# Performance work log

Hardware: AMD Instinct MI355X
Metric: run time of the kernel (lower is better)

Reference implementation:

```python
import jax, jax.numpy as jnp
import numpy as np

B, NT, DIM, H = 8, 1024, 768, 12
HD = DIM // H
SCALE = HD ** -0.5


def setup_inputs() -> dict:
    key = jax.random.key(0)
    ks = jax.random.split(key, 9)
    s = DIM ** -0.5
    return {
        "tfeat": jax.random.normal(ks[0], (B, NT, DIM), jnp.float32),
        "wq": jax.random.normal(ks[1], (DIM, DIM), jnp.float32) * s,
        "bq": jnp.zeros((DIM,), jnp.float32),
        "wk": jax.random.normal(ks[2], (DIM, DIM), jnp.float32) * s,
        "bk": jnp.zeros((DIM,), jnp.float32),
        "wv": jax.random.normal(ks[3], (DIM, DIM), jnp.float32) * s,
        "bv": jnp.zeros((DIM,), jnp.float32),
        "wp": jax.random.normal(ks[4], (DIM, DIM), jnp.float32) * s,
        "bp": jnp.zeros((DIM,), jnp.float32),
    }


def reference(tfeat, wq, bq, wk, bk, wv, bv, wp, bp):
    # Linear stores weight [out, in]; y = x @ W^T + b
    def split_heads(x):  # [B,Nt,C] -> [B,H,Nt,hd]
        b, n, c = x.shape
        return x.reshape(b, n, H, HD).transpose(0, 2, 1, 3)

    q = split_heads(tfeat @ wq.T + bq)
    k = split_heads(tfeat @ wk.T + bk)
    v = split_heads(tfeat @ wv.T + bv)
    # [B,H,Nt,Nt]
    attn = jax.nn.softmax(jnp.einsum('bhqd,bhkd->bhqk', q, k) * SCALE, axis=-1)
    # dropout is identity in eval mode
    x = jnp.einsum('bhqk,bhkd->bhqd', attn, v)
    x = x.transpose(0, 2, 1, 3).reshape(tfeat.shape)
    x = x @ wp.T + bp
    return (x, attn)
```

## Files before the change

### kernel.cpp

```cpp
#include <hip/hip_runtime.h>
#include <hip/hip_bf16.h>
#include <math.h>

#define B_    8
#define NT_   1024
#define DIM_  768
#define H_    12
#define HD_   64
#define SCALE_ 0.125f

typedef _Float16 half8  __attribute__((ext_vector_type(8)));
typedef float    floatx4 __attribute__((ext_vector_type(4)));

__global__ void cvt_f32_f16(const float* __restrict__ in,
                            _Float16* __restrict__ out, int n) {
  int i = blockIdx.x * 256 + threadIdx.x;
  if (i < n) out[i] = (_Float16)in[i];
}

template<bool F32OUT>
__global__ __launch_bounds__(256) void gemm_bt(
    const _Float16* __restrict__ A, const _Float16* __restrict__ Bt,
    const float* __restrict__ bias, _Float16* __restrict__ outh,
    float* __restrict__ outf, int M, int N, int K)
{
  __shared__ _Float16 As[64][40];
  __shared__ _Float16 Bs[64][40];
  const int t    = threadIdx.x;
  const int w    = t >> 6, lane = t & 63;
  const int quad = lane >> 4, l16 = lane & 15;
  const int wm   = (w >> 1) * 32, wn = (w & 1) * 32;
  const int m0   = blockIdx.x * 64, n0 = blockIdx.y * 64;
  const int lrow = t >> 2, lcol = (t & 3) * 8;

  floatx4 acc[2][2] = {};

  for (int k0 = 0; k0 < K; k0 += 32) {
    uint4 av = *(const uint4*)(A  + (size_t)(m0 + lrow) * K + k0 + lcol);
    uint4 bv = *(const uint4*)(Bt + (size_t)(n0 + lrow) * K + k0 + lcol);
    __syncthreads();
    *(uint4*)(&As[lrow][lcol]) = av;
    *(uint4*)(&Bs[lrow][lcol]) = bv;
    __syncthreads();
    half8 a0 = *(const half8*)(&As[wm      + l16][quad * 8]);
    half8 a1 = *(const half8*)(&As[wm + 16 + l16][quad * 8]);
    half8 b0 = *(const half8*)(&Bs[wn      + l16][quad * 8]);
    half8 b1 = *(const half8*)(&Bs[wn + 16 + l16][quad * 8]);
    acc[0][0] = __builtin_amdgcn_mfma_f32_16x16x32_f16(a0, b0, acc[0][0], 0, 0, 0);
    acc[0][1] = __builtin_amdgcn_mfma_f32_16x16x32_f16(a0, b1, acc[0][1], 0, 0, 0);
    acc[1][0] = __builtin_amdgcn_mfma_f32_16x16x32_f16(a1, b0, acc[1][0], 0, 0, 0);
    acc[1][1] = __builtin_amdgcn_mfma_f32_16x16x32_f16(a1, b1, acc[1][1], 0, 0, 0);
  }

  for (int i = 0; i < 2; i++)
    for (int j = 0; j < 2; j++)
      for (int r = 0; r < 4; r++) {
        int row = m0 + wm + i * 16 + quad * 4 + r;
        int col = n0 + wn + j * 16 + l16;
        float v = acc[i][j][r] + bias[col];
        if (F32OUT) outf[(size_t)row * N + col] = v;
        else        outh[(size_t)row * N + col] = (_Float16)v;
      }
}

__global__ __launch_bounds__(256) void attn_kernel(
    const _Float16* __restrict__ Qh, const _Float16* __restrict__ Kh,
    const _Float16* __restrict__ Vh, float* __restrict__ attn_out,
    _Float16* __restrict__ Xh)
{
  __shared__ _Float16 Qs[64][72];
  __shared__ _Float16 Ks[64][72];
  __shared__ _Float16 Vt[64][72];
  __shared__ _Float16 Ps[64][72];

  const int t    = threadIdx.x;
  const int w    = t >> 6, lane = t & 63;
  const int quad = lane >> 4, l16 = lane & 15;
  const int qt = blockIdx.x, h = blockIdx.y, b = blockIdx.z;
  const int q0 = qt * 64;

  const _Float16* Qb = Qh + ((size_t)b * NT_) * DIM_ + h * HD_;
  const _Float16* Kb = Kh + ((size_t)b * NT_) * DIM_ + h * HD_;
  const _Float16* Vb = Vh + ((size_t)b * NT_) * DIM_ + h * HD_;

  const int lrow = t >> 2;
  const int lcol = (t & 3) * 16;

  *(uint4*)(&Qs[lrow][lcol])     = *(const uint4*)(Qb + (size_t)(q0 + lrow) * DIM_ + lcol);
  *(uint4*)(&Qs[lrow][lcol + 8]) = *(const uint4*)(Qb + (size_t)(q0 + lrow) * DIM_ + lcol + 8);

  float m_run[4], l_run[4];
#pragma unroll
  for (int r = 0; r < 4; r++) { m_run[r] = -INFINITY; l_run[r] = 0.0f; }

  for (int kt = 0; kt < 16; kt++) {
    __syncthreads();
    *(uint4*)(&Ks[lrow][lcol])     = *(const uint4*)(Kb + (size_t)(kt * 64 + lrow) * DIM_ + lcol);
    *(uint4*)(&Ks[lrow][lcol + 8]) = *(const uint4*)(Kb + (size_t)(kt * 64 + lrow) * DIM_ + lcol + 8);
    __syncthreads();

    floatx4 s[4] = {};
#pragma unroll
    for (int ks = 0; ks < 2; ks++) {
      half8 a = *(const half8*)(&Qs[w * 16 + l16][ks * 32 + quad * 8]);
#pragma unroll
      for (int j = 0; j < 4; j++) {
        half8 bk = *(const half8*)(&Ks[j * 16 + l16][ks * 32 + quad * 8]);
        s[j] = __builtin_amdgcn_mfma_f32_16x16x32_f16(a, bk, s[j], 0, 0, 0);
      }
    }
#pragma unroll
    for (int r = 0; r < 4; r++) {
      float tm = -INFINITY;
#pragma unroll
      for (int j = 0; j < 4; j++) tm = fmaxf(tm, s[j][r] * SCALE_);
      for (int off = 1; off < 16; off <<= 1)
        tm = fmaxf(tm, __shfl_xor(tm, off, 64));
      float nm = fmaxf(m_run[r], tm);
      float ts = 0.0f;
#pragma unroll
      for (int j = 0; j < 4; j++) ts += expf(s[j][r] * SCALE_ - nm);
      for (int off = 1; off < 16; off <<= 1)
        ts += __shfl_xor(ts, off, 64);
      l_run[r] = l_run[r] * expf(m_run[r] - nm) + ts;
      m_run[r] = nm;
    }
  }

  float inv_l[4];
#pragma unroll
  for (int r = 0; r < 4; r++) inv_l[r] = 1.0f / l_run[r];

  floatx4 oacc[4] = {};
  float* attn_b = attn_out + ((size_t)(b * H_ + h) * NT_ + q0) * NT_;

  for (int kt = 0; kt < 16; kt++) {
    __syncthreads();
    *(uint4*)(&Ks[lrow][lcol])     = *(const uint4*)(Kb + (size_t)(kt * 64 + lrow) * DIM_ + lcol);
    *(uint4*)(&Ks[lrow][lcol + 8]) = *(const uint4*)(Kb + (size_t)(kt * 64 + lrow) * DIM_ + lcol + 8);
    {
      alignas(16) _Float16 vh[16];
      *(uint4*)(vh)     = *(const uint4*)(Vb + (size_t)(kt * 64 + lrow) * DIM_ + lcol);
      *(uint4*)(vh + 8) = *(const uint4*)(Vb + (size_t)(kt * 64 + lrow) * DIM_ + lcol + 8);
#pragma unroll
      for (int c = 0; c < 16; c++) Vt[lcol + c][lrow] = vh[c];
    }
    __syncthreads();

    floatx4 s[4] = {};
#pragma unroll
    for (int ks = 0; ks < 2; ks++) {
      half8 a = *(const half8*)(&Qs[w * 16 + l16][ks * 32 + quad * 8]);
#pragma unroll
      for (int j = 0; j < 4; j++) {
        half8 bk = *(const half8*)(&Ks[j * 16 + l16][ks * 32 + quad * 8]);
        s[j] = __builtin_amdgcn_mfma_f32_16x16x32_f16(a, bk, s[j], 0, 0, 0);
      }
    }

#pragma unroll
    for (int j = 0; j < 4; j++)
#pragma unroll
      for (int r = 0; r < 4; r++) {
        float p = expf(s[j][r] * SCALE_ - m_run[r]) * inv_l[r];
        int qr = w * 16 + quad * 4 + r;
        attn_b[(size_t)qr * NT_ + kt * 64 + j * 16 + l16] = p;
        Ps[qr][j * 16 + l16] = (_Float16)p;
      }

#pragma unroll
    for (int ks = 0; ks < 2; ks++) {
      half8 pa = *(const half8*)(&Ps[w * 16 + l16][ks * 32 + quad * 8]);
#pragma unroll
      for (int j2 = 0; j2 < 4; j2++) {
        half8 bv = *(const half8*)(&Vt[j2 * 16 + l16][ks * 32 + quad * 8]);
        oacc[j2] = __builtin_amdgcn_mfma_f32_16x16x32_f16(pa, bv, oacc[j2], 0, 0, 0);
      }
    }
  }

#pragma unroll
  for (int j2 = 0; j2 < 4; j2++)
#pragma unroll
    for (int r = 0; r < 4; r++) {
      int qr = q0 + w * 16 + quad * 4 + r;
      Xh[((size_t)b * NT_ + qr) * DIM_ + h * HD_ + j2 * 16 + l16] = (_Float16)oacc[j2][r];
    }
}

extern "C" void kernel_launch(void* const* d_in, const int* in_sizes, int n_in,
                              void* d_out, int out_size, void* d_ws, size_t ws_size,
                              hipStream_t stream) {
  const float* tfeat = (const float*)d_in[0];
  const float* wq    = (const float*)d_in[1];
  const float* bq    = (const float*)d_in[2];
  const float* wk    = (const float*)d_in[3];
  const float* bk    = (const float*)d_in[4];
  const float* wv    = (const float*)d_in[5];
  const float* bv    = (const float*)d_in[6];
  const float* wp    = (const float*)d_in[7];
  const float* bp    = (const float*)d_in[8];
  float* out = (float*)d_out;

  const size_t T = (size_t)B_ * NT_ * DIM_;
  const size_t W = (size_t)DIM_ * DIM_;

  _Float16* ws  = (_Float16*)d_ws;
  _Float16* tfh = ws;
  _Float16* wqh = ws + T;
  _Float16* wkh = ws + T + W;
  _Float16* wvh = ws + T + 2 * W;
  _Float16* wph = ws + T + 3 * W;
  _Float16* Qh  = ws + T + 4 * W;
  _Float16* Kh  = Qh + T;
  _Float16* Vh  = Kh + T;
  _Float16* Xh  = Vh + T;

  cvt_f32_f16<<<(int)((T + 255) / 256), 256, 0, stream>>>(tfeat, tfh, (int)T);
  cvt_f32_f16<<<(int)((W + 255) / 256), 256, 0, stream>>>(wq, wqh, (int)W);
  cvt_f32_f16<<<(int)((W + 255) / 256), 256, 0, stream>>>(wk, wkh, (int)W);
  cvt_f32_f16<<<(int)((W + 255) / 256), 256, 0, stream>>>(wv, wvh, (int)W);
  cvt_f32_f16<<<(int)((W + 255) / 256), 256, 0, stream>>>(wp, wph, (int)W);

  dim3 gg(8192 / 64, 768 / 64);
  gemm_bt<false><<<gg, 256, 0, stream>>>(tfh, wqh, bq, Qh, nullptr, 8192, 768, 768);
  gemm_bt<false><<<gg, 256, 0, stream>>>(tfh, wkh, bk, Kh, nullptr, 8192, 768, 768);
  gemm_bt<false><<<gg, 256, 0, stream>>>(tfh, wvh, bv, Vh, nullptr, 8192, 768, 768);

  attn_kernel<<<dim3(NT_ / 64, H_, B_), 256, 0, stream>>>(Qh, Kh, Vh, out + T, Xh);

  gemm_bt<true><<<gg, 256, 0, stream>>>(Xh, wph, bp, nullptr, out, 8192, 768, 768);
}
```

Before: 711.4 us.

## Fuse QKV GEMMs into 128x128 LDS-DMA GEMM, exp2 softmax, vectorized casts

Replaces the 64x64 GEMM with a 128x128-tile kernel that loads global data straight into LDS through global_load_lds, and merges the Q, K and V projections into one launch by relying on the contiguous workspace layout of wq/wk/wv. The attention kernel now keeps Q fragments in registers instead of LDS. Softmax uses exp2 with a prescaled log2e constant and folds 1/l into the exponent via log2(l). The f32-to-f16 casts are vectorized to four elements per thread. Together these aim to cut launch count, raise GEMM data reuse and reduce transcendental cost, at the price of more registers and an unpadded LDS layout that may cause bank conflicts.

```diff
diff --git a/kernel.cpp b/kernel.cpp
--- a/kernel.cpp
+++ b/kernel.cpp
@@ -1,5 +1,4 @@
 #include <hip/hip_runtime.h>
-#include <hip/hip_bf16.h>
 #include <math.h>
 
 #define B_    8
@@ -8,59 +7,99 @@
 #define H_    12
 #define HD_   64
 #define SCALE_ 0.125f
+#define T_ELEMS 6291456UL
 
 typedef _Float16 half8  __attribute__((ext_vector_type(8)));
+typedef _Float16 half4v __attribute__((ext_vector_type(4)));
 typedef float    floatx4 __attribute__((ext_vector_type(4)));
 
-__global__ void cvt_f32_f16(const float* __restrict__ in,
-                            _Float16* __restrict__ out, int n) {
+#if __has_builtin(__builtin_amdgcn_exp2f)
+#define EXP2F(x) __builtin_amdgcn_exp2f(x)
+#else
+#define EXP2F(x) exp2f(x)
+#endif
+
+#define GLD16(gp, lp) __builtin_amdgcn_global_load_lds( \
+    (const __attribute__((address_space(1))) unsigned int*)(gp), \
+    (__attribute__((address_space(3))) unsigned int*)(lp), 16, 0, 0)
+
+__global__ void cvt4(const float* __restrict__ in, _Float16* __restrict__ out,
+                     int n4) {
   int i = blockIdx.x * 256 + threadIdx.x;
-  if (i < n) out[i] = (_Float16)in[i];
-}
-
-template<bool F32OUT>
-__global__ __launch_bounds__(256) void gemm_bt(
+  if (i < n4) {
+    float4 v = ((const float4*)in)[i];
+    half4v h = { (_Float16)v.x, (_Float16)v.y, (_Float16)v.z, (_Float16)v.w };
+    *(half4v*)(out + 4 * (size_t)i) = h;
+  }
+}
+
+template<int MODE>
+__global__ __launch_bounds__(256) void gemm128(
     const _Float16* __restrict__ A, const _Float16* __restrict__ Bt,
-    const float* __restrict__ bias, _Float16* __restrict__ outh,
-    float* __restrict__ outf, int M, int N, int K)
+    const float* __restrict__ b0_, const float* __restrict__ b1_,
+    const float* __restrict__ b2_, _Float16* __restrict__ outh,
+    float* __restrict__ outf, int K)
 {
-  __shared__ _Float16 As[64][40];
-  __shared__ _Float16 Bs[64][40];
+  __shared__ _Float16 As[128 * 32];
+  __shared__ _Float16 Bs[128 * 32];
   const int t    = threadIdx.x;
   const int w    = t >> 6, lane = t & 63;
   const int quad = lane >> 4, l16 = lane & 15;
-  const int wm   = (w >> 1) * 32, wn = (w & 1) * 32;
-  const int m0   = blockIdx.x * 64, n0 = blockIdx.y * 64;
-  const int lrow = t >> 2, lcol = (t & 3) * 8;
-
-  floatx4 acc[2][2] = {};
+  const int wm   = (w >> 1) * 64, wn = (w & 1) * 64;
+  const int m0   = blockIdx.x * 128, n0 = blockIdx.y * 128;
+
+  const _Float16* gA = A  + (size_t)(m0 + (t >> 2)) * K + (t & 3) * 8;
+  const _Float16* gB = Bt + (size_t)(n0 + (t >> 2)) * K + (t & 3) * 8;
+  _Float16* lA = As + w * 512;
+  _Float16* lB = Bs + w * 512;
+  const size_t rowK = (size_t)64 * K;
+
+  floatx4 acc[4][4] = {};
 
   for (int k0 = 0; k0 < K; k0 += 32) {
-    uint4 av = *(const uint4*)(A  + (size_t)(m0 + lrow) * K + k0 + lcol);
-    uint4 bv = *(const uint4*)(Bt + (size_t)(n0 + lrow) * K + k0 + lcol);
-    __syncthreads();
-    *(uint4*)(&As[lrow][lcol]) = av;
-    *(uint4*)(&Bs[lrow][lcol]) = bv;
-    __syncthreads();
-    half8 a0 = *(const half8*)(&As[wm      + l16][quad * 8]);
-    half8 a1 = *(const half8*)(&As[wm + 16 + l16][quad * 8]);
-    half8 b0 = *(const half8*)(&Bs[wn      + l16][quad * 8]);
-    half8 b1 = *(const half8*)(&Bs[wn + 16 + l16][quad * 8]);
-    acc[0][0] = __builtin_amdgcn_mfma_f32_16x16x32_f16(a0, b0, acc[0][0], 0, 0, 0);
-    acc[0][1] = __builtin_amdgcn_mfma_f32_16x16x32_f16(a0, b1, acc[0][1], 0, 0, 0);
-    acc[1][0] = __builtin_amdgcn_mfma_f32_16x16x32_f16(a1, b0, acc[1][0], 0, 0, 0);
-    acc[1][1] = __builtin_amdgcn_mfma_f32_16x16x32_f16(a1, b1, acc[1][1], 0, 0, 0);
-  }
-
-  for (int i = 0; i < 2; i++)
-    for (int j = 0; j < 2; j++)
+    __syncthreads();
+    GLD16(gA + k0,        lA);
+    GLD16(gA + rowK + k0, lA + 2048);
+    GLD16(gB + k0,        lB);
+    GLD16(gB + rowK + k0, lB + 2048);
+    __syncthreads();
+
+    half8 af[4], bf[4];
+#pragma unroll
+    for (int i = 0; i < 4; i++)
+      af[i] = *(const half8*)(As + (wm + i * 16 + l16) * 32 + quad * 8);
+#pragma unroll
+    for (int j = 0; j < 4; j++)
+      bf[j] = *(const half8*)(Bs + (wn + j * 16 + l16) * 32 + quad * 8);
+#pragma unroll
+    for (int i = 0; i < 4; i++)
+#pragma unroll
+      for (int j = 0; j < 4; j++)
+        acc[i][j] = __builtin_amdgcn_mfma_f32_16x16x32_f16(af[i], bf[j],
+                                                           acc[i][j], 0, 0, 0);
+  }
+
+  const int sel = (MODE == 0) ? (n0 / 768) : 0;
+  const float* bb = (MODE == 0)
+                      ? (sel == 0 ? b0_ : (sel == 1 ? b1_ : b2_))
+                      : b0_;
+#pragma unroll
+  for (int j = 0; j < 4; j++) {
+    const int col = n0 + wn + j * 16 + l16;
+    const int cl  = col - sel * 768;
+    const float bv = bb[cl];
+#pragma unroll
+    for (int i = 0; i < 4; i++)
+#pragma unroll
       for (int r = 0; r < 4; r++) {
-        int row = m0 + wm + i * 16 + quad * 4 + r;
-        int col = n0 + wn + j * 16 + l16;
-        float v = acc[i][j][r] + bias[col];
-        if (F32OUT) outf[(size_t)row * N + col] = v;
-        else        outh[(size_t)row * N + col] = (_Float16)v;
-      }
+        const int row = m0 + wm + i * 16 + quad * 4 + r;
+        const float v = acc[i][j][r] + bv;
+        if (MODE == 0)
+          outh[(size_t)sel * T_ELEMS + (size_t)row * 768 + cl] = (_Float16)v;
+        else
+          outf[(size_t)row * 768 + col] = v;
+      }
+  }
 }
 
 __global__ __launch_bounds__(256) void attn_kernel(
@@ -68,7 +107,6 @@
     const _Float16* __restrict__ Vh, float* __restrict__ attn_out,
     _Float16* __restrict__ Xh)
 {
-  __shared__ _Float16 Qs[64][72];
   __shared__ _Float16 Ks[64][72];
   __shared__ _Float16 Vt[64][72];
   __shared__ _Float16 Ps[64][72];
@@ -86,9 +124,14 @@
   const int lrow = t >> 2;
   const int lcol = (t & 3) * 16;
 
-  *(uint4*)(&Qs[lrow][lcol])     = *(const uint4*)(Qb + (size_t)(q0 + lrow) * DIM_ + lcol);
-  *(uint4*)(&Qs[lrow][lcol + 8]) = *(const uint4*)(Qb + (size_t)(q0 + lrow) * DIM_ + lcol + 8);
-
+  half8 qf[2];
+  {
+    const _Float16* qr = Qb + (size_t)(q0 + w * 16 + l16) * DIM_ + quad * 8;
+    qf[0] = *(const half8*)(qr);
+    qf[1] = *(const half8*)(qr + 32);
+  }
+
+  const float C2 = 0.18033688011112042f;
   float m_run[4], l_run[4];
 #pragma unroll
   for (int r = 0; r < 4; r++) { m_run[r] = -INFINITY; l_run[r] = 0.0f; }
@@ -102,34 +145,31 @@
     floatx4 s[4] = {};
 #pragma unroll
     for (int ks = 0; ks < 2; ks++) {
-      half8 a = *(const half8*)(&Qs[w * 16 + l16][ks * 32 + quad * 8]);
 #pragma unroll
       for (int j = 0; j < 4; j++) {
         half8 bk = *(const half8*)(&Ks[j * 16 + l16][ks * 32 + quad * 8]);
-        s[j] = __builtin_amdgcn_mfma_f32_16x16x32_f16(a, bk, s[j], 0, 0, 0);
+        s[j] = __builtin_amdgcn_mfma_f32_16x16x32_f16(qf[ks], bk, s[j], 0, 0, 0);
       }
     }
 #pragma unroll
     for (int r = 0; r < 4; r++) {
-      float tm = -INFINITY;
-#pragma unroll
-      for (int j = 0; j < 4; j++) tm = fmaxf(tm, s[j][r] * SCALE_);
+      float tm = fmaxf(fmaxf(s[0][r], s[1][r]), fmaxf(s[2][r], s[3][r]));
       for (int off = 1; off < 16; off <<= 1)
         tm = fmaxf(tm, __shfl_xor(tm, off, 64));
-      float nm = fmaxf(m_run[r], tm);
-      float ts = 0.0f;
-#pragma unroll
-      for (int j = 0; j < 4; j++) ts += expf(s[j][r] * SCALE_ - nm);
+      const float nm  = fmaxf(m_run[r], tm);
+      const float nmc = nm * C2;
+      float ts = EXP2F(fmaf(s[0][r], C2, -nmc)) + EXP2F(fmaf(s[1][r], C2, -nmc))
+               + EXP2F(fmaf(s[2][r], C2, -nmc)) + EXP2F(fmaf(s[3][r], C2, -nmc));
       for (int off = 1; off < 16; off <<= 1)
         ts += __shfl_xor(ts, off, 64);
-      l_run[r] = l_run[r] * expf(m_run[r] - nm) + ts;
+      l_run[r] = l_run[r] * EXP2F((m_run[r] - nm) * C2) + ts;
       m_run[r] = nm;
     }
   }
 
-  float inv_l[4];
-#pragma unroll
-  for (int r = 0; r < 4; r++) inv_l[r] = 1.0f / l_run[r];
+  float mb[4];
+#pragma unroll
+  for (int r = 0; r < 4; r++) mb[r] = m_run[r] * C2 + log2f(l_run[r]);
 
   floatx4 oacc[4] = {};
   float* attn_b = attn_out + ((size_t)(b * H_ + h) * NT_ + q0) * NT_;
@@ -150,11 +190,10 @@
     floatx4 s[4] = {};
 #pragma unroll
     for (int ks = 0; ks < 2; ks++) {
-      half8 a = *(const half8*)(&Qs[w * 16 + l16][ks * 32 + quad * 8]);
 #pragma unroll
       for (int j = 0; j < 4; j++) {
         half8 bk = *(const half8*)(&Ks[j * 16 + l16][ks * 32 + quad * 8]);
-        s[j] = __builtin_amdgcn_mfma_f32_16x16x32_f16(a, bk, s[j], 0, 0, 0);
+        s[j] = __builtin_amdgcn_mfma_f32_16x16x32_f16(qf[ks], bk, s[j], 0, 0, 0);
       }
     }
 
@@ -162,8 +201,8 @@
     for (int j = 0; j < 4; j++)
 #pragma unroll
       for (int r = 0; r < 4; r++) {
-        float p = expf(s[j][r] * SCALE_ - m_run[r]) * inv_l[r];
-        int qr = w * 16 + quad * 4 + r;
+        const float p = EXP2F(fmaf(s[j][r], C2, -mb[r]));
+        const int qr = w * 16 + quad * 4 + r;
         attn_b[(size_t)qr * NT_ + kt * 64 + j * 16 + l16] = p;
         Ps[qr][j * 16 + l16] = (_Float16)p;
       }
@@ -183,7 +222,7 @@
   for (int j2 = 0; j2 < 4; j2++)
 #pragma unroll
     for (int r = 0; r < 4; r++) {
-      int qr = q0 + w * 16 + quad * 4 + r;
+      const int qr = q0 + w * 16 + quad * 4 + r;
       Xh[((size_t)b * NT_ + qr) * DIM_ + h * HD_ + j2 * 16 + l16] = (_Float16)oacc[j2][r];
     }
 }
@@ -202,7 +241,7 @@
   const float* bp    = (const float*)d_in[8];
   float* out = (float*)d_out;
 
-  const size_t T = (size_t)B_ * NT_ * DIM_;
+  const size_t T = T_ELEMS;
   const size_t W = (size_t)DIM_ * DIM_;
 
   _Float16* ws  = (_Float16*)d_ws;
@@ -216,18 +255,15 @@
   _Float16* Vh  = Kh + T;
   _Float16* Xh  = Vh + T;
 
-  cvt_f32_f16<<<(int)((T + 255) / 256), 256, 0, stream>>>(tfeat, tfh, (int)T);
-  cvt_f32_f16<<<(int)((W + 255) / 256), 256, 0, stream>>>(wq, wqh, (int)W);
-  cvt_f32_f16<<<(int)((W + 255) / 256), 256, 0, stream>>>(wk, wkh, (int)W);
-  cvt_f32_f16<<<(int)((W + 255) / 256), 256, 0, stream>>>(wv, wvh, (int)W);
-  cvt_f32_f16<<<(int)((W + 255) / 256), 256, 0, stream>>>(wp, wph, (int)W);
-
-  dim3 gg(8192 / 64, 768 / 64);
-  gemm_bt<false><<<gg, 256, 0, stream>>>(tfh, wqh, bq, Qh, nullptr, 8192, 768, 768);
-  gemm_bt<false><<<gg, 256, 0, stream>>>(tfh, wkh, bk, Kh, nullptr, 8192, 768, 768);
-  gemm_bt<false><<<gg, 256, 0, stream>>>(tfh, wvh, bv, Vh, nullptr, 8192, 768, 768);
+  cvt4<<<(int)(T / 4 / 256), 256, 0, stream>>>(tfeat, tfh, (int)(T / 4));
+  cvt4<<<(int)(W / 4 / 256), 256, 0, stream>>>(wq, wqh, (int)(W / 4));
+  cvt4<<<(int)(W / 4 / 256), 256, 0, stream>>>(wk, wkh, (int)(W / 4));
+  cvt4<<<(int)(W / 4 / 256), 256, 0, stream>>>(wv, wvh, (int)(W / 4));
+  cvt4<<<(int)(W / 4 / 256), 256, 0, stream>>>(wp, wph, (int)(W / 4));
+
+  gemm128<0><<<dim3(64, 18), 256, 0, stream>>>(tfh, wqh, bq, bk, bv, Qh, nullptr, 768);
 
   attn_kernel<<<dim3(NT_ / 64, H_, B_), 256, 0, stream>>>(Qh, Kh, Vh, out + T, Xh);
 
-  gemm_bt<true><<<gg, 256, 0, stream>>>(Xh, wph, bp, nullptr, out, 8192, 768, 768);
-}
+  gemm128<1><<<dim3(64, 6), 256, 0, stream>>>(Xh, wph, bp, nullptr, nullptr, nullptr, out, 768);
+}
```

Measured after the change: 632.5 us. 1.12x faster.
